# Optimization experiments

Measured on AMD Instinct MI355X. Metric: run time of the kernel, lower is better.

Reference implementation:

```python
import jax, jax.numpy as jnp
from jax import lax
import numpy as np

B, C, H, W = 64, 1, 512, 512
N_MULT = 1  # len(mul_approx_func_arr)


def setup_inputs() -> dict:
    key = jax.random.key(0)
    k1, = jax.random.split(key, 1)
    # image-like pixel inputs in [0, 255)
    inp = jax.random.uniform(k1, (B, C, H, W), dtype=jnp.float32) * 255.0
    # Gaussian kernel params, tiled per multiplier variant (as in __init__)
    base = jnp.array([1.0, 2.0, 1.0, 2.0, 4.0, 2.0, 1.0, 2.0, 1.0], dtype=jnp.float32) / 16.0
    weight = jnp.tile(base[None, :], (N_MULT, 1))            # [N_MULT, 9]
    weight_factor = jnp.full((N_MULT, 1), 16.0, jnp.float32)  # [N_MULT, 1]
    return {"input": inp, "weight": weight, "weight_factor": weight_factor}


def _ste_quantize(x):
    # QuantizeGrad: forward = clamp(round(x), 0.001, inf); backward = identity (STE)
    q = jnp.clip(jnp.round(x), 0.001, None)
    return x + lax.stop_gradient(q - x)


def reference(input, weight, weight_factor):
    # in-place .data clamp (no grad through the clamp itself)
    wc_data = weight + lax.stop_gradient(jnp.clip(weight, 0.001, 0.999) - weight)
    wf_data = weight_factor + lax.stop_gradient(jnp.clip(weight_factor, 1.001, 254.999) - weight_factor)
    # hardtanh clamps (identity in-range after the data clamp)
    wc = jnp.clip(wc_data, 0.0, 1.0)
    wf = jnp.clip(wf_data, 1.0, 255.0)
    outs = []
    for ii in range(N_MULT):
        # weight_rounded: 9-element 3x3 kernel via STE quantization
        wr = _ste_quantize(wc[ii] * wf[ii])          # [9]
        kernel = wr.reshape(1, 1, 3, 3)
        # accurate_mult_only summed over the 9 taps == 3x3 conv, padding=1.
        # The approximate-multiplier forward value (mul_wrapper, emulated here as
        # exact multiply, index=1 accurate) is written into x.data, so forward
        # value and gradient path coincide under this emulation.
        y = lax.conv_general_dilated(
            input, kernel.astype(input.dtype),
            window_strides=(1, 1), padding=((1, 1), (1, 1)),
            dimension_numbers=("NCHW", "OIHW", "NCHW"))
        outs.append(y)
    # torch.stack(output, 0): [N_MULT, B, C, H, W]
    return jnp.stack(outs, 0)
```

## Files before the change

### kernel.cpp

```cpp
#include <hip/hip_runtime.h>


#define BB 64
#define HH 512
#define WW 512
#define W4 (WW / 4)
#define RR 8

typedef float vfloat4 __attribute__((ext_vector_type(4)));

__global__ __launch_bounds__(256) void gauss3x3_kernel(
    const float* __restrict__ in,
    const float* __restrict__ wgt,
    const float* __restrict__ wfac,
    float* __restrict__ out)
{
    float wf = fminf(fmaxf(wfac[0], 1.001f), 254.999f);
    float k[9];
#pragma unroll
    for (int i = 0; i < 9; ++i) {
        float wc = fminf(fmaxf(wgt[i], 0.001f), 0.999f);
        k[i] = fmaxf(rintf(wc * wf), 0.001f);
    }

    const int tid   = blockIdx.x * blockDim.x + threadIdx.x;
    const int lane  = threadIdx.x & 63;
    const int x4    = tid & (W4 - 1);
    const int strip = (tid >> 7) & (HH / RR - 1);
    const int b     = tid >> 13;
    if (b >= BB) return;

    const int y0 = strip * RR;
    const int x0 = x4 * 4;
    const float* img  = in  + (size_t)b * HH * WW;
    float*       outp = out + (size_t)b * HH * WW;

    float4 acc[RR];
#pragma unroll
    for (int i = 0; i < RR; ++i) acc[i] = make_float4(0.f, 0.f, 0.f, 0.f);

#pragma unroll
    for (int j = 0; j < RR + 2; ++j) {
        const int ry = y0 - 1 + j;
        float4 c = make_float4(0.f, 0.f, 0.f, 0.f);
        float  l = 0.f, r = 0.f;
        if (ry >= 0 && ry < HH) {
            const float* row = img + (size_t)ry * WW;
            c = *(const float4*)(row + x0);
            l = __shfl_up(c.w, 1);
            r = __shfl_down(c.x, 1);
            if (lane == 0)
                l = (x0 > 0) ? row[x0 - 1] : 0.f;
            if (lane == 63)
                r = (x0 + 4 < WW) ? row[x0 + 4] : 0.f;
        }
#pragma unroll
        for (int t = 0; t < 3; ++t) {
            const int i = j - t;
            if (i >= 0 && i < RR) {
                const float kl = k[t * 3 + 0];
                const float kc = k[t * 3 + 1];
                const float kr = k[t * 3 + 2];
                acc[i].x = fmaf(kl, l,   fmaf(kc, c.x, fmaf(kr, c.y, acc[i].x)));
                acc[i].y = fmaf(kl, c.x, fmaf(kc, c.y, fmaf(kr, c.z, acc[i].y)));
                acc[i].z = fmaf(kl, c.y, fmaf(kc, c.z, fmaf(kr, c.w, acc[i].z)));
                acc[i].w = fmaf(kl, c.z, fmaf(kc, c.w, fmaf(kr, r,   acc[i].w)));
            }
        }
    }

#pragma unroll
    for (int i = 0; i < RR; ++i) {
        vfloat4* dst = (vfloat4*)(outp + (size_t)(y0 + i) * WW + x0);
        vfloat4 v = { acc[i].x, acc[i].y, acc[i].z, acc[i].w };
        __builtin_nontemporal_store(v, dst);
    }
}

extern "C" void kernel_launch(void* const* d_in, const int* in_sizes, int n_in,
                              void* d_out, int out_size, void* d_ws, size_t ws_size,
                              hipStream_t stream) {
    const float* in   = (const float*)d_in[0];
    const float* wgt  = (const float*)d_in[1];
    const float* wfac = (const float*)d_in[2];
    float* out = (float*)d_out;

    const int total = BB * (HH / RR) * W4;
    const int block = 256;
    const int grid  = total / block;
    gauss3x3_kernel<<<grid, block, 0, stream>>>(in, wgt, wfac, out);
}
```

Before: 114.0 us.

## Double rows per thread, swizzle block order, and store rows as they complete

Each thread now computes 16 output rows instead of 8, which cuts the halo row re-reads between strips. Block IDs are remapped so that consecutive blocks are spread across 8 interleaved groups, likely to spread work across XCDs or memory channels. Each output row is stored as soon as its last tap row is accumulated, rather than all rows at the end, and the accumulator zero-init is dropped by starting each row with a plain multiply. The cost is half as many threads for the whole problem and more work per thread, which may lower latency hiding.

Result: slower. 117.4 us (+3.0%).

```diff
diff --git a/kernel.cpp b/kernel.cpp
--- a/kernel.cpp
+++ b/kernel.cpp
@@ -5,7 +5,10 @@
 #define HH 512
 #define WW 512
 #define W4 (WW / 4)
-#define RR 8
+#define RR 16
+#define NSTRIP (HH / RR)
+#define NTHREADS (BB * NSTRIP * W4)
+#define GRID (NTHREADS / 256)
 
 typedef float vfloat4 __attribute__((ext_vector_type(4)));
 
@@ -23,11 +26,14 @@
         k[i] = fmaxf(rintf(wc * wf), 0.001f);
     }
 
-    const int tid   = blockIdx.x * blockDim.x + threadIdx.x;
+    const int bid = blockIdx.x;
+    const int swz = (bid & 7) * (GRID / 8) + (bid >> 3);
+    const int tid = swz * 256 + (int)threadIdx.x;
+
     const int lane  = threadIdx.x & 63;
     const int x4    = tid & (W4 - 1);
-    const int strip = (tid >> 7) & (HH / RR - 1);
-    const int b     = tid >> 13;
+    const int strip = (tid >> 7) & (NSTRIP - 1);
+    const int b     = tid >> 12;
     if (b >= BB) return;
 
     const int y0 = strip * RR;
@@ -36,8 +42,6 @@
     float*       outp = out + (size_t)b * HH * WW;
 
     float4 acc[RR];
-#pragma unroll
-    for (int i = 0; i < RR; ++i) acc[i] = make_float4(0.f, 0.f, 0.f, 0.f);
 
 #pragma unroll
     for (int j = 0; j < RR + 2; ++j) {
@@ -54,26 +58,30 @@
             if (lane == 63)
                 r = (x0 + 4 < WW) ? row[x0 + 4] : 0.f;
         }
-#pragma unroll
-        for (int t = 0; t < 3; ++t) {
-            const int i = j - t;
-            if (i >= 0 && i < RR) {
-                const float kl = k[t * 3 + 0];
-                const float kc = k[t * 3 + 1];
-                const float kr = k[t * 3 + 2];
-                acc[i].x = fmaf(kl, l,   fmaf(kc, c.x, fmaf(kr, c.y, acc[i].x)));
-                acc[i].y = fmaf(kl, c.x, fmaf(kc, c.y, fmaf(kr, c.z, acc[i].y)));
-                acc[i].z = fmaf(kl, c.y, fmaf(kc, c.z, fmaf(kr, c.w, acc[i].z)));
-                acc[i].w = fmaf(kl, c.z, fmaf(kc, c.w, fmaf(kr, r,   acc[i].w)));
-            }
+
+        if (j < RR) {
+            acc[j].x = k[0] * l   + k[1] * c.x + k[2] * c.y;
+            acc[j].y = k[0] * c.x + k[1] * c.y + k[2] * c.z;
+            acc[j].z = k[0] * c.y + k[1] * c.z + k[2] * c.w;
+            acc[j].w = k[0] * c.z + k[1] * c.w + k[2] * r;
         }
-    }
-
-#pragma unroll
-    for (int i = 0; i < RR; ++i) {
-        vfloat4* dst = (vfloat4*)(outp + (size_t)(y0 + i) * WW + x0);
-        vfloat4 v = { acc[i].x, acc[i].y, acc[i].z, acc[i].w };
-        __builtin_nontemporal_store(v, dst);
+        if (j >= 1 && (j - 1) < RR) {
+            const int i = j - 1;
+            acc[i].x = fmaf(k[3], l,   fmaf(k[4], c.x, fmaf(k[5], c.y, acc[i].x)));
+            acc[i].y = fmaf(k[3], c.x, fmaf(k[4], c.y, fmaf(k[5], c.z, acc[i].y)));
+            acc[i].z = fmaf(k[3], c.y, fmaf(k[4], c.z, fmaf(k[5], c.w, acc[i].z)));
+            acc[i].w = fmaf(k[3], c.z, fmaf(k[4], c.w, fmaf(k[5], r,   acc[i].w)));
+        }
+        if (j >= 2) {
+            const int i = j - 2;
+            acc[i].x = fmaf(k[6], l,   fmaf(k[7], c.x, fmaf(k[8], c.y, acc[i].x)));
+            acc[i].y = fmaf(k[6], c.x, fmaf(k[7], c.y, fmaf(k[8], c.z, acc[i].y)));
+            acc[i].z = fmaf(k[6], c.y, fmaf(k[7], c.z, fmaf(k[8], c.w, acc[i].z)));
+            acc[i].w = fmaf(k[6], c.z, fmaf(k[7], c.w, fmaf(k[8], r,   acc[i].w)));
+            vfloat4* dst = (vfloat4*)(outp + (size_t)(y0 + i) * WW + x0);
+            vfloat4 v = { acc[i].x, acc[i].y, acc[i].z, acc[i].w };
+            __builtin_nontemporal_store(v, dst);
+        }
     }
 }
 
@@ -85,8 +93,5 @@
     const float* wfac = (const float*)d_in[2];
     float* out = (float*)d_out;
 
-    const int total = BB * (HH / RR) * W4;
-    const int block = 256;
-    const int grid  = total / block;
-    gauss3x3_kernel<<<grid, block, 0, stream>>>(in, wgt, wfac, out);
+    gauss3x3_kernel<<<GRID, 256, 0, stream>>>(in, wgt, wfac, out);
 }
```
